# Kernel tuning notes

Measured on AMD Instinct MI355X. Metric: run time of the kernel, lower is better.

Reference implementation:

```python
import jax, jax.numpy as jnp
import numpy as np
from jax import lax

# PRPN (Parse-Read-Predict Network), eval mode (all dropout off, BatchNorm in eval
# with running stats mean=0/var=1, rmask=ones). Submodule math follows the upstream
# yikangshen/PRPN implementation vendored by jiant: ParsingNetwork (conv gate stack,
# hard hardtanh memory gates with cumprod over slots), ReadingNetwork (masked-softmax
# attention over nslots memory + LayerNorm LSTM cell, shift-append memory update),
# PredictNetwork (attention over prediction memory, res=0 -> Linear+BN+Tanh head).

T, B, V, D, H, S, L, NL = 192, 32, 50000, 384, 384, 15, 5, 2
RES = 0.1
G4 = 4 * H
BN_SC = np.float32(1.0 / np.sqrt(1.0 + 1e-5))   # eval BatchNorm with mean=0, var=1
INV_SQRT_H = np.float32(1.0 / np.sqrt(H))


def _layer_norm(x, g, b, eps=1e-6):
    # torch-style LayerNorm with unbiased std (x.std(-1))
    mu = jnp.mean(x, -1, keepdims=True)
    var = jnp.sum((x - mu) ** 2, -1, keepdims=True) / (x.shape[-1] - 1)
    return g * (x - mu) / (jnp.sqrt(var) + eps) + b


def _msoftmax(logits, gate, eps=1e-8):
    # blocks.softmax: exp-normalize then multiply by (soft) gate mask before sum
    e = jnp.exp(logits - jnp.max(logits, -1, keepdims=True)) * gate
    return e / (jnp.sum(e, -1, keepdims=True) + eps)


def _forward(input_ids, emb_w, pconv1_w, pconv1_b, pbn_g, pbn_b, pconv2_w, pconv2_b,
             r_wih, r_bih, r_whh, r_bhh, r_lnih_g, r_lnih_b, r_lnhh_g, r_lnhh_b,
             r_lnc_g, r_lnc_b, r_proj_w, r_proj_b,
             p_proj_w, p_proj_b, p_ffd_w, p_ffd_b, p_bn_g, p_bn_b):
    emb = emb_w[input_ids]                                        # (T,B,D)

    # ---- ParsingNetwork ----
    x = jnp.concatenate([jnp.zeros((L, B, D), emb.dtype), emb], 0)  # (T+L,B,D), zero history
    xc = jnp.transpose(x, (1, 2, 0))                              # (B,D,T+L)
    h1 = lax.conv_general_dilated(xc, pconv1_w, (1,), 'VALID',
                                  dimension_numbers=('NCH', 'OIH', 'NCH'))
    h1 = h1 + pconv1_b[None, :, None]
    h1 = jax.nn.relu(pbn_g[None, :, None] * h1 * BN_SC + pbn_b[None, :, None])  # (B,H,T)
    half = H // 2
    # Conv1d(nhid, 2, 1, groups=2): channel 0 from first half, channel 1 from second
    gate = jax.nn.sigmoid(jnp.einsum('bct,c->bt', h1[:, :half], pconv2_w[0]) + pconv2_b[0])
    gate_next = jax.nn.sigmoid(jnp.einsum('bct,c->bt', h1[:, half:], pconv2_w[1]) + pconv2_b[1])
    cum = jnp.concatenate([jnp.full((B, S), 1e9, gate.dtype), gate], 1)  # init cum_gate = +inf
    gate_hat = jnp.stack([cum[:, S - k:S - k + T] for k in range(S)], 2)  # (B,T,S)

    def mem_gate(g):  # hard gates: (hardtanh((g-ghat)/res*2+1)+1)/2, cumprod over slots
        u = (jnp.clip((g[:, :, None] - gate_hat) / RES * 2.0 + 1.0, -1.0, 1.0) + 1.0) * 0.5
        return jnp.cumprod(u, axis=2)

    mg = jnp.transpose(mem_gate(gate), (1, 0, 2))                 # (T,B,S)
    mgn = jnp.transpose(mem_gate(gate_next), (1, 0, 2))           # (T,B,S)

    # ---- per-timestep Read / Predict-attention loop ----
    def step(carry, xs):
        mem_h, mem_c, pmem = carry       # (NL,B,S,H),(NL,B,S,H),(B,S,H)
        e_t, mg_t, mgn_t = xs
        h = e_t
        nh, nc = [], []
        for j in range(NL):
            mh, mc = mem_h[j], mem_c[j]
            key_j = jnp.concatenate([h, mh[:, -1]], -1) @ r_proj_w[j].T + r_proj_b[j]
            att = _msoftmax(jnp.einsum('bsh,bh->bs', mh, key_j) * INV_SQRT_H, mg_t)
            sel_h = jnp.einsum('bs,bsh->bh', att, mh)
            sel_c = jnp.einsum('bs,bsh->bh', att, mc)
            gates = (_layer_norm(h @ r_wih[j].T + r_bih[j], r_lnih_g[j], r_lnih_b[j])
                     + _layer_norm(sel_h @ r_whh[j].T + r_bhh[j], r_lnhh_g[j], r_lnhh_b[j]))
            i_g, f_g, c_g, o_g = jnp.split(gates, 4, axis=-1)
            c_new = jax.nn.sigmoid(f_g) * sel_c + jax.nn.sigmoid(i_g) * jnp.tanh(c_g)
            h_new = jax.nn.sigmoid(o_g) * jnp.tanh(_layer_norm(c_new, r_lnc_g[j], r_lnc_b[j]))
            nh.append(jnp.concatenate([mh[:, 1:], h_new[:, None]], 1))
            nc.append(jnp.concatenate([mc[:, 1:], c_new[:, None]], 1))
            h = h_new
        pkey = jnp.concatenate([h, pmem[:, -1]], -1) @ p_proj_w.T + p_proj_b
        patt = _msoftmax(jnp.einsum('bsh,bh->bs', pmem, pkey) * INV_SQRT_H, mgn_t)
        sel = jnp.einsum('bs,bsh->bh', patt, pmem)
        pmem_new = jnp.concatenate([pmem[:, 1:], h[:, None]], 1)
        return (jnp.stack(nh), jnp.stack(nc), pmem_new), (h, sel)

    carry0 = (jnp.zeros((NL, B, S, H), emb.dtype),
              jnp.zeros((NL, B, S, H), emb.dtype),
              jnp.zeros((B, S, H), emb.dtype))
    _, (out_h, out_sel) = lax.scan(step, carry0, (emb, mg, mgn))

    # ---- PredictNetwork head (res=0): Linear(2H->D) + BN(eval) + Tanh ----
    flat = jnp.concatenate([out_h.reshape(T * B, H), out_sel.reshape(T * B, H)], -1)
    y = flat @ p_ffd_w.T + p_ffd_b
    y = jnp.tanh(p_bn_g * y * BN_SC + p_bn_b)
    return y.reshape(T, B, D)


def setup_inputs() -> dict:
    key = jax.random.key(0)
    ks = iter(jax.random.split(key, 16))

    def rn(shape, s=0.05):
        return jax.random.normal(next(ks), shape, dtype=jnp.float32) * s

    return {
        "input_ids": jax.random.randint(next(ks), (T, B), 0, V),
        "emb_w": rn((V, D), 0.01),
        "pconv1_w": rn((H, D, L + 1)),
        "pconv1_b": jnp.zeros((H,), jnp.float32),
        "pbn_g": jnp.ones((H,), jnp.float32),
        "pbn_b": jnp.zeros((H,), jnp.float32),
        "pconv2_w": rn((2, H // 2)),
        "pconv2_b": jnp.zeros((2,), jnp.float32),
        "r_wih": rn((NL, G4, D)),
        "r_bih": jnp.zeros((NL, G4), jnp.float32),
        "r_whh": rn((NL, G4, H)),
        "r_bhh": jnp.zeros((NL, G4), jnp.float32),
        "r_lnih_g": jnp.ones((NL, G4), jnp.float32),
        "r_lnih_b": jnp.zeros((NL, G4), jnp.float32),
        "r_lnhh_g": jnp.ones((NL, G4), jnp.float32),
        "r_lnhh_b": jnp.zeros((NL, G4), jnp.float32),
        "r_lnc_g": jnp.ones((NL, H), jnp.float32),
        "r_lnc_b": jnp.zeros((NL, H), jnp.float32),
        "r_proj_w": rn((NL, H, D + H)),
        "r_proj_b": jnp.zeros((NL, H), jnp.float32),
        "p_proj_w": rn((H, 2 * H)),
        "p_proj_b": jnp.zeros((H,), jnp.float32),
        "p_ffd_w": rn((D, 2 * H)),
        "p_ffd_b": jnp.zeros((D,), jnp.float32),
        "p_bn_g": jnp.ones((D,), jnp.float32),
        "p_bn_b": jnp.zeros((D,), jnp.float32),
    }


def reference(input_ids, emb_w, pconv1_w, pconv1_b, pbn_g, pbn_b, pconv2_w, pconv2_b,
              r_wih, r_bih, r_whh, r_bhh, r_lnih_g, r_lnih_b, r_lnhh_g, r_lnhh_b,
              r_lnc_g, r_lnc_b, r_proj_w, r_proj_b,
              p_proj_w, p_proj_b, p_ffd_w, p_ffd_b, p_bn_g, p_bn_b):
    out = _forward(input_ids, emb_w, pconv1_w, pconv1_b, pbn_g, pbn_b, pconv2_w, pconv2_b,
                   r_wih, r_bih, r_whh, r_bhh, r_lnih_g, r_lnih_b, r_lnhh_g, r_lnhh_b,
                   r_lnc_g, r_lnc_b, r_proj_w, r_proj_b,
                   p_proj_w, p_proj_b, p_ffd_w, p_ffd_b, p_bn_g, p_bn_b)
    mask = input_ids != 0
    return out, mask
```

## Files before the change

### kernel.cpp

```cpp
#include <hip/hip_runtime.h>


#define TT 192
#define TB 6144

constexpr size_t O_EMB    = 0;
constexpr size_t O_IH0LN  = 2359296;
constexpr size_t O_KEY0E  = 11796480;
constexpr size_t O_MG     = 14155776;
constexpr size_t O_MGN    = 14247936;
constexpr size_t O_H1     = 14340096;
constexpr size_t O_P0S    = 14340096;
constexpr size_t O_P1S    = 14389248;
constexpr size_t O_IH1RAW = 14438400;
constexpr size_t O_KEY1H  = 14536704;
constexpr size_t O_KEY0MH = 14561280;
constexpr size_t O_KEY1MH = 14573568;
constexpr size_t O_PKEYH  = 14585856;
constexpr size_t O_PKEYMH = 14610432;
constexpr size_t O_HNEW0  = 14635008;
constexpr size_t O_HNEW1  = 14647296;
constexpr size_t O_BAR    = 14671872;
constexpr size_t O_DEADEND= 14675968;
constexpr size_t O_GATEA  = 16699392;
constexpr size_t O_GATEB  = 16705536;
constexpr size_t O_OUTHS  = 16711680;
constexpr size_t O_MEMH0  = 21430272;
constexpr size_t O_MEMC0  = 21614592;
constexpr size_t O_MEMH1  = 21798912;
constexpr size_t O_MEMC1  = 21983232;
constexpr size_t O_PMEM   = 22167552;
constexpr size_t O_P0     = 22351872;
constexpr size_t O_P1     = 23089152;
constexpr size_t O_STATEEND = 23826432;

#define L0F 0
#define L1F 512
#define PRF 1024
#define G0F 1536
#define G1F 3072

__device__ __forceinline__ float sigmoidf(float x) { return 1.f / (1.f + expf(-x)); }

__device__ __forceinline__ float ldx(const float* p) {
  return __hip_atomic_load(p, __ATOMIC_RELAXED, __HIP_MEMORY_SCOPE_AGENT);
}
__device__ __forceinline__ void stx(float* p, float v) {
  __hip_atomic_store(p, v, __ATOMIC_RELAXED, __HIP_MEMORY_SCOPE_AGENT);
}
__device__ __forceinline__ float2 ldx2(const float* p) {
  unsigned long long v = __hip_atomic_load((const unsigned long long*)p,
                                           __ATOMIC_RELAXED, __HIP_MEMORY_SCOPE_AGENT);
  return __builtin_bit_cast(float2, v);
}
__device__ __forceinline__ void stx2(float* p, float2 v) {
  __hip_atomic_store((unsigned long long*)p, __builtin_bit_cast(unsigned long long, v),
                     __ATOMIC_RELAXED, __HIP_MEMORY_SCOPE_AGENT);
}
__device__ __forceinline__ int ldi(const int* p) {
  return __hip_atomic_load(p, __ATOMIC_RELAXED, __HIP_MEMORY_SCOPE_AGENT);
}
__device__ __forceinline__ void sti(int* p, int v) {
  __hip_atomic_store(p, v, __ATOMIC_RELAXED, __HIP_MEMORY_SCOPE_AGENT);
}

constexpr float BN_SC = 0.9999950000374997f;
constexpr float INV_SQRT_H = 0.05103103630798288f;

__device__ __forceinline__ float blockSum(float v, float* red) {
#pragma unroll
  for (int off = 32; off > 0; off >>= 1) v += __shfl_down(v, off, 64);
  __syncthreads();
  if ((threadIdx.x & 63) == 0) red[threadIdx.x >> 6] = v;
  __syncthreads();
  return red[0] + red[1] + red[2] + red[3];
}

__device__ __forceinline__ float2 wred2(float a, float b) {
#pragma unroll
  for (int off = 32; off > 0; off >>= 1) {
    a += __shfl_xor(a, off, 64);
    b += __shfl_xor(b, off, 64);
  }
  return make_float2(a, b);
}

__global__ __launch_bounds__(256) void k_zero(float* p, int n) {
  int i = blockIdx.x * 256 + threadIdx.x;
  int stride = gridDim.x * 256;
  for (; i < n; i += stride) p[i] = 0.f;
}

__global__ __launch_bounds__(256) void k_emb(const int* ids, const float* emb_w,
                                             float* emb, float* out) {
  size_t idx = (size_t)blockIdx.x * 256 + threadIdx.x;
  size_t stride = (size_t)gridDim.x * 256;
  for (size_t i = idx; i < (size_t)TB * 384; i += stride) {
    size_t tb = i / 384, d = i - tb * 384;
    int id = ids[tb];
    emb[i] = emb_w[(size_t)id * 384 + d];
    if (i < TB) out[(size_t)TB * 384 + i] = (ids[i] != 0) ? 1.f : 0.f;
  }
}

__global__ __launch_bounds__(256) void k_conv(const float* emb, const float* W1, const float* cbias,
                                              const float* bng, const float* bnb, float* h1) {
  __shared__ float As[32][68];
  __shared__ float Bs[32][68];
  int n0 = blockIdx.x * 64, m0 = blockIdx.y * 64;
  int tid = threadIdx.x;
  float acc[4][4] = {};
  int mi = tid >> 3, kq = tid & 7;
  int ni = tid >> 2, kb = tid & 3;
  for (int kk = 0; kk < 2304; kk += 32) {
    int kc = kk / 384, dbase = kk - kc * 384;
    __syncthreads();
#pragma unroll
    for (int p = 0; p < 2; ++p) {
      int m = m0 + mi + 32 * p;
      int b = m / 192, t = m - b * 192;
      int tt = t + kc - 5;
      float4 v = {0.f, 0.f, 0.f, 0.f};
      if (tt >= 0) v = *(const float4*)(emb + ((size_t)tt * 32 + b) * 384 + dbase + kq * 4);
      As[kq * 4 + 0][mi + 32 * p] = v.x; As[kq * 4 + 1][mi + 32 * p] = v.y;
      As[kq * 4 + 2][mi + 32 * p] = v.z; As[kq * 4 + 3][mi + 32 * p] = v.w;
    }
#pragma unroll
    for (int i = 0; i < 8; ++i) {
      int d = dbase + kb * 8 + i;
      Bs[kb * 8 + i][ni] = W1[(size_t)(n0 + ni) * 2304 + d * 6 + kc];
    }
    __syncthreads();
    int ty = tid >> 4, tx = tid & 15;
#pragma unroll
    for (int k = 0; k < 32; ++k) {
      float4 a = *(const float4*)(&As[k][ty * 4]);
      float4 bv = *(const float4*)(&Bs[k][tx * 4]);
      acc[0][0] += a.x * bv.x; acc[0][1] += a.x * bv.y; acc[0][2] += a.x * bv.z; acc[0][3] += a.x * bv.w;
      acc[1][0] += a.y * bv.x; acc[1][1] += a.y * bv.y; acc[1][2] += a.y * bv.z; acc[1][3] += a.y * bv.w;
      acc[2][0] += a.z * bv.x; acc[2][1] += a.z * bv.y; acc[2][2] += a.z * bv.z; acc[2][3] += a.z * bv.w;
      acc[3][0] += a.w * bv.x; acc[3][1] += a.w * bv.y; acc[3][2] += a.w * bv.z; acc[3][3] += a.w * bv.w;
    }
  }
  int ty = tid >> 4, tx = tid & 15;
#pragma unroll
  for (int i = 0; i < 4; ++i) {
    int m = m0 + ty * 4 + i;
#pragma unroll
    for (int j = 0; j < 4; ++j) {
      int n = n0 + tx * 4 + j;
      float v = acc[i][j] + cbias[n];
      v = bng[n] * v * BN_SC + bnb[n];
      h1[(size_t)m * 384 + n] = fmaxf(v, 0.f);
    }
  }
}

__global__ __launch_bounds__(256) void k_gate(const float* h1, const float* w2, const float* b2,
                                              float* gA, float* gB) {
  __shared__ float red[8];
  int bt = blockIdx.x, tid = threadIdx.x;
  float v0 = 0.f, v1 = 0.f;
  if (tid < 192) {
    v0 = h1[(size_t)bt * 384 + tid] * w2[tid];
    v1 = h1[(size_t)bt * 384 + 192 + tid] * w2[192 + tid];
  }
  float s0 = blockSum(v0, red);
  float s1 = blockSum(v1, red);
  if (tid == 0) {
    gA[bt] = 1.f / (1.f + expf(-(s0 + b2[0])));
    gB[bt] = 1.f / (1.f + expf(-(s1 + b2[1])));
  }
}

__global__ __launch_bounds__(256) void k_mg(const float* gA, const float* gB, float* mg, float* mgn) {
  int idx = blockIdx.x * 256 + threadIdx.x;
  if (idx >= TB) return;
  int t = idx >> 5, b = idx & 31;
  float g = gA[b * 192 + t], gn = gB[b * 192 + t];
  float p = 1.f, pn = 1.f;
  for (int k = 0; k < 15; ++k) {
    float ghat = (k <= t) ? gA[b * 192 + t - k] : 1e9f;
    float u = fminf(fmaxf((g - ghat) / 0.1f * 2.f + 1.f, -1.f), 1.f);
    float un = fminf(fmaxf((gn - ghat) / 0.1f * 2.f + 1.f, -1.f), 1.f);
    p *= (u + 1.f) * 0.5f;
    pn *= (un + 1.f) * 0.5f;
    mg[(size_t)idx * 15 + k] = p;
    mgn[(size_t)idx * 15 + k] = pn;
  }
}

__global__ __launch_bounds__(256) void k_gemm(const float* A, int lda, const float* W, int ldw,
                                              const float* bias, float* Cf, int ldc, int K, int mode,
                                              const float* bng, const float* bnb, float* Cb) {
  __shared__ float As[32][68];
  __shared__ float Bs[32][68];
  int n0 = blockIdx.x * 64, m0 = blockIdx.y * 64;
  int tid = threadIdx.x;
  float acc[4][4] = {};
  int mi = tid >> 3, kq = tid & 7;
  int ni = tid >> 2, kb = tid & 3;
  for (int kk = 0; kk < K; kk += 32) {
    __syncthreads();
#pragma unroll
    for (int p = 0; p < 2; ++p) {
      int m = m0 + mi + 32 * p;
      float4 v = *(const float4*)(A + (size_t)m * lda + kk + kq * 4);
      As[kq * 4 + 0][mi + 32 * p] = v.x; As[kq * 4 + 1][mi + 32 * p] = v.y;
      As[kq * 4 + 2][mi + 32 * p] = v.z; As[kq * 4 + 3][mi + 32 * p] = v.w;
    }
    {
      const float* wp = W + (size_t)(n0 + ni) * ldw + kk + kb * 8;
      float4 q0 = *(const float4*)(wp);
      float4 q1 = *(const float4*)(wp + 4);
      Bs[kb * 8 + 0][ni] = q0.x; Bs[kb * 8 + 1][ni] = q0.y;
      Bs[kb * 8 + 2][ni] = q0.z; Bs[kb * 8 + 3][ni] = q0.w;
      Bs[kb * 8 + 4][ni] = q1.x; Bs[kb * 8 + 5][ni] = q1.y;
      Bs[kb * 8 + 6][ni] = q1.z; Bs[kb * 8 + 7][ni] = q1.w;
    }
    __syncthreads();
    int ty = tid >> 4, tx = tid & 15;
#pragma unroll
    for (int k = 0; k < 32; ++k) {
      float4 a = *(const float4*)(&As[k][ty * 4]);
      float4 bv = *(const float4*)(&Bs[k][tx * 4]);
      acc[0][0] += a.x * bv.x; acc[0][1] += a.x * bv.y; acc[0][2] += a.x * bv.z; acc[0][3] += a.x * bv.w;
      acc[1][0] += a.y * bv.x; acc[1][1] += a.y * bv.y; acc[1][2] += a.y * bv.z; acc[1][3] += a.y * bv.w;
      acc[2][0] += a.z * bv.x; acc[2][1] += a.z * bv.y; acc[2][2] += a.z * bv.z; acc[2][3] += a.z * bv.w;
      acc[3][0] += a.w * bv.x; acc[3][1] += a.w * bv.y; acc[3][2] += a.w * bv.z; acc[3][3] += a.w * bv.w;
    }
  }
  int ty = tid >> 4, tx = tid & 15;
#pragma unroll
  for (int i = 0; i < 4; ++i) {
    int m = m0 + ty * 4 + i;
#pragma unroll
    for (int j = 0; j < 4; ++j) {
      int n = n0 + tx * 4 + j;
      float v = acc[i][j];
      if (bias) v += bias[n];
      if (mode == 0) Cf[(size_t)m * ldc + n] = v;
      else Cb[(size_t)m * ldc + n] = tanhf(bng[n] * v * BN_SC + bnb[n]);
    }
  }
}

__global__ __launch_bounds__(256) void k_ln_rows(float* X, const float* g, const float* bt) {
  __shared__ float red[8];
  float* x = X + (size_t)blockIdx.x * 1536;
  int tid = threadIdx.x;
  float ps = 0.f;
  for (int i = tid; i < 1536; i += 256) ps += x[i];
  float mu = blockSum(ps, red) * (1.f / 1536.f);
  ps = 0.f;
  for (int i = tid; i < 1536; i += 256) { float d = x[i] - mu; ps += d * d; }
  float inv = 1.f / (sqrtf(blockSum(ps, red) * (1.f / 1535.f)) + 1e-6f);
  for (int i = tid; i < 1536; i += 256) x[i] = g[i] * (x[i] - mu) * inv + bt[i];
}

struct ScanArgs {
  float* ws;
  const float *r_whh, *r_bhh, *r_lnhh_g, *r_lnhh_b, *r_lnih_g, *r_lnih_b;
  const float *r_lnc_g, *r_lnc_b, *r_wih, *r_bih, *r_proj_w, *r_proj_b;
  const float *p_proj_w, *p_proj_b;
};

struct GJob { const float* W; int ldw; int koff; const float* bias; float* dst; int rstride; int ncols; };

__device__ __forceinline__ void resolveJob(const GJob* J, int col, const float*& W, int& ldw, int& koff,
                                           const float*& bias, float*& dst, int& rstride, int& cc) {
  int c = col;
#pragma unroll
  for (int j = 0; j < 4; ++j) {
    if (c < J[j].ncols) {
      W = J[j].W; ldw = J[j].ldw; koff = J[j].koff; bias = J[j].bias;
      dst = J[j].dst; rstride = J[j].rstride; cc = c; return;
    }
    c -= J[j].ncols;
  }
  W = J[0].W; ldw = J[0].ldw; koff = J[0].koff; bias = J[0].bias;
  dst = J[0].dst; rstride = J[0].rstride; cc = 0;
}

__device__ __forceinline__ void stage_x(const float* src, float* xs) {
  const int tid = threadIdx.x;
  for (int j2 = tid; j2 < 6144; j2 += 256) {
    int j = j2 * 2;
    int bb = j / 384, kk = j - bb * 384;
    float2 v = ldx2(src + j);
    xs[bb * 385 + kk] = v.x; xs[bb * 385 + kk + 1] = v.y;
  }
}

__device__ void gemv_run(const GJob* J, int cbase, int ncols, const float* xs, float* red) {
  const int tid = threadIdx.x;
  const int b = tid & 31, cg = tid >> 5;
  float xr[48];
  const float* xp = xs + b * 385 + cg * 48;
#pragma unroll
  for (int q = 0; q < 48; ++q) xr[q] = xp[q];
  for (int ch = 0; ch < ncols; ch += 21) {
    const int nch = min(21, ncols - ch);
    for (int ci = 0; ci < nch; ++ci) {
      const float* W; int ldw, koff; const float* bias; float* dst; int rstride; int cc;
      resolveJob(J, cbase + ch + ci, W, ldw, koff, bias, dst, rstride, cc);
      const float* wr = W + (size_t)cc * ldw + koff + cg * 48;
      float a = 0.f;
#pragma unroll
      for (int q = 0; q < 12; ++q) {
        float4 w = *(const float4*)(wr + q * 4);
        a += w.x * xr[q * 4 + 0] + w.y * xr[q * 4 + 1]
           + w.z * xr[q * 4 + 2] + w.w * xr[q * 4 + 3];
      }
      a += __shfl_down(a, 32, 64);
      if ((cg & 1) == 0) red[((cg >> 1) * nch + ci) * 33 + b] = a;
    }
    __syncthreads();
    const int pairs = nch * 32;
    for (int pi = tid; pi < pairs; pi += 256) {
      int bb = pi / nch, ci = pi - bb * nch;
      float s = red[(0 * nch + ci) * 33 + bb] + red[(1 * nch + ci) * 33 + bb]
              + red[(2 * nch + ci) * 33 + bb] + red[(3 * nch + ci) * 33 + bb];
      const float* W; int ldw, koff; const float* bias; float* dst; int rstride; int cc;
      resolveJob(J, cbase + ch + ci, W, ldw, koff, bias, dst, rstride, cc);
      if (bias) s += bias[cc];
      stx(dst + (size_t)bb * rstride + cc, s);
    }
    __syncthreads();
  }
}

__device__ __forceinline__ void wave_attn(const float* memh, const float* klds, const float* mgp,
                                          int t, int lane, float (&att)[15]) {
  const int g = lane >> 2, l = lane & 3;
  float part = 0.f;
  if (g < 15) {
    const float* mh = memh + ((t + g) % 15) * 384 + l;
#pragma unroll 8
    for (int k = 0; k < 96; ++k) part += mh[4 * k] * klds[l + 4 * k];
  }
  part += __shfl_xor(part, 1, 64);
  part += __shfl_xor(part, 2, 64);
  float logit[15];
#pragma unroll
  for (int s = 0; s < 15; ++s) logit[s] = __shfl(part, 4 * s, 64) * INV_SQRT_H;
  float m = logit[0];
#pragma unroll
  for (int s = 1; s < 15; ++s) m = fmaxf(m, logit[s]);
  float sum = 0.f;
#pragma unroll
  for (int s = 0; s < 15; ++s) { att[s] = expf(logit[s] - m) * mgp[s]; sum += att[s]; }
  float inv = 1.f / (sum + 1e-8f);
#pragma unroll
  for (int s = 0; s < 15; ++s) att[s] *= inv;
}

__device__ void l0_loop(int b, int lane, float* klds, const ScanArgs& A, int* bar) {
  float* ws = A.ws;
  float* memh = ws + O_MEMH0 + (size_t)b * 5760;
  float* memc = ws + O_MEMC0 + (size_t)b * 5760;
  float* mir  = ws + O_P0 + (size_t)b * 23040;
  const float* stg = ws + O_P0S + (size_t)b * 1536;
  const int* p1 = bar + G0F + lane * 16;
  const int* p2 = bar + G0F + (64 + (lane & 31)) * 16;
  for (int t = 0; t < 192; ++t) {
    const size_t tb = (size_t)t * 32 + b;
    float2 ih[12];
#pragma unroll
    for (int j = 0; j < 12; ++j)
      ih[j] = *(const float2*)(ws + O_IH0LN + tb * 1536 + 2 * lane + 128 * j);
    float2 kE[3];
#pragma unroll
    for (int j = 0; j < 3; ++j)
      kE[j] = *(const float2*)(ws + O_KEY0E + tb * 384 + 2 * lane + 128 * j);
    while (true) {
      int a = ldi(p1);
      int c = (lane < 32) ? ldi(p2) : 0x7fffffff;
      if (__all(a >= t && c >= t)) break;
      __builtin_amdgcn_s_sleep(1);
    }
    float2 fresh[12];
#pragma unroll
    for (int j = 0; j < 12; ++j) fresh[j] = ldx2(stg + 2 * lane + 128 * j);
#pragma unroll
    for (int j = 0; j < 3; ++j) {
      float2 c2 = ldx2(ws + O_KEY0MH + (size_t)b * 384 + 2 * lane + 128 * j);
      *(float2*)(klds + 2 * lane + 128 * j) = make_float2(kE[j].x + c2.x, kE[j].y + c2.y);
    }
    float att[15];
    wave_attn(memh, klds, ws + O_MG + tb * 15, t, lane, att);
    float2 acc[12];
#pragma unroll
    for (int j = 0; j < 12; ++j) {
      float2 bb = *(const float2*)(A.r_bhh + 2 * lane + 128 * j);
      acc[j] = make_float2(bb.x + att[14] * fresh[j].x, bb.y + att[14] * fresh[j].y);
    }
#pragma unroll
    for (int s = 0; s < 14; ++s) {
      const float* P = mir + ((t + s) % 15) * 1536;
      float a = att[s];
#pragma unroll
      for (int j = 0; j < 12; ++j) {
        float2 p = *(const float2*)(P + 2 * lane + 128 * j);
        acc[j].x += a * p.x; acc[j].y += a * p.y;
      }
    }
    float2 selc[3];
#pragma unroll
    for (int j = 0; j < 3; ++j) selc[j] = make_float2(0.f, 0.f);
#pragma unroll
    for (int s = 0; s < 15; ++s) {
      const float* C = memc + ((t + s) % 15) * 384;
      float a = att[s];
#pragma unroll
      for (int j = 0; j < 3; ++j) {
        float2 p = *(const float2*)(C + 2 * lane + 128 * j);
        selc[j].x += a * p.x; selc[j].y += a * p.y;
      }
    }
    float s1 = 0.f, s2 = 0.f;
#pragma unroll
    for (int j = 0; j < 12; ++j) {
      s1 += acc[j].x + acc[j].y;
      s2 += acc[j].x * acc[j].x + acc[j].y * acc[j].y;
    }
    float2 r = wred2(s1, s2);
    float mu = r.x * (1.f / 1536.f);
    float inv = 1.f / (sqrtf(fmaxf(r.y - r.x * mu, 0.f) * (1.f / 1535.f)) + 1e-6f);
    const float* hg = A.r_lnhh_g;
    const float* hb = A.r_lnhh_b;
    float2 cn[3], og[3];
#pragma unroll
    for (int jj = 0; jj < 3; ++jj) {
      const int d = 2 * lane + 128 * jj;
      float2 gi, gf, gc, go;
      { float2 g2 = *(const float2*)(hg + d), b2 = *(const float2*)(hb + d);
        gi.x = ih[jj].x + g2.x * (acc[jj].x - mu) * inv + b2.x;
        gi.y = ih[jj].y + g2.y * (acc[jj].y - mu) * inv + b2.y; }
      { float2 g2 = *(const float2*)(hg + 384 + d), b2 = *(const float2*)(hb + 384 + d);
        gf.x = ih[3 + jj].x + g2.x * (acc[3 + jj].x - mu) * inv + b2.x;
        gf.y = ih[3 + jj].y + g2.y * (acc[3 + jj].y - mu) * inv + b2.y; }
      { float2 g2 = *(const float2*)(hg + 768 + d), b2 = *(const float2*)(hb + 768 + d);
        gc.x = ih[6 + jj].x + g2.x * (acc[6 + jj].x - mu) * inv + b2.x;
        gc.y = ih[6 + jj].y + g2.y * (acc[6 + jj].y - mu) * inv + b2.y; }
      { float2 g2 = *(const float2*)(hg + 1152 + d), b2 = *(const float2*)(hb + 1152 + d);
        go.x = ih[9 + jj].x + g2.x * (acc[9 + jj].x - mu) * inv + b2.x;
        go.y = ih[9 + jj].y + g2.y * (acc[9 + jj].y - mu) * inv + b2.y; }
      cn[jj].x = sigmoidf(gf.x) * selc[jj].x + sigmoidf(gi.x) * tanhf(gc.x);
      cn[jj].y = sigmoidf(gf.y) * selc[jj].y + sigmoidf(gi.y) * tanhf(gc.y);
      og[jj] = go;
    }
    s1 = 0.f; s2 = 0.f;
#pragma unroll
    for (int jj = 0; jj < 3; ++jj) {
      s1 += cn[jj].x + cn[jj].y;
      s2 += cn[jj].x * cn[jj].x + cn[jj].y * cn[jj].y;
    }
    r = wred2(s1, s2);
    float mu_c = r.x * (1.f / 384.f);
    float inv_c = 1.f / (sqrtf(fmaxf(r.y - r.x * mu_c, 0.f) * (1.f / 383.f)) + 1e-6f);
    const int slot = t % 15;
    const int pslot = (t + 14) % 15;
#pragma unroll
    for (int jj = 0; jj < 3; ++jj) {
      const int d = 2 * lane + 128 * jj;
      float2 lg2 = *(const float2*)(A.r_lnc_g + d), lb2 = *(const float2*)(A.r_lnc_b + d);
      float2 hn;
      hn.x = sigmoidf(og[jj].x) * tanhf(lg2.x * (cn[jj].x - mu_c) * inv_c + lb2.x);
      hn.y = sigmoidf(og[jj].y) * tanhf(lg2.y * (cn[jj].y - mu_c) * inv_c + lb2.y);
      *(float2*)(memh + slot * 384 + d) = hn;
      *(float2*)(memc + slot * 384 + d) = cn[jj];
      stx2(ws + O_HNEW0 + (size_t)b * 384 + d, hn);
    }
#pragma unroll
    for (int j = 0; j < 12; ++j)
      *(float2*)(mir + pslot * 1536 + 2 * lane + 128 * j) = fresh[j];
    asm volatile("s_waitcnt vmcnt(0)" ::: "memory");
    if (lane == 0) sti(bar + L0F + b * 16, t + 1);
  }
}

__device__ void l1_loop(int b, int lane, float* klds, const ScanArgs& A, int* bar) {
  float* ws = A.ws;
  float* memh = ws + O_MEMH1 + (size_t)b * 5760;
  float* memc = ws + O_MEMC1 + (size_t)b * 5760;
  float* mir  = ws + O_P1 + (size_t)b * 23040;
  const float* stg = ws + O_P1S + (size_t)b * 1536;
  const float* hg = A.r_lnhh_g + 1536;
  const float* hb = A.r_lnhh_b + 1536;
  const float* igp = A.r_lnih_g + 1536;
  const float* ibp = A.r_lnih_b + 1536;
  const float* bhh = A.r_bhh + 1536;
  const float* lcg = A.r_lnc_g + 384;
  const float* lcb = A.r_lnc_b + 384;
  const int* p1 = bar + G0F + lane * 16;
  const int* p2 = bar + G0F + (64 + (lane & 31)) * 16;
  const int* p3 = bar + G1F + lane * 16;
  for (int t = 0; t < 192; ++t) {
    while (true) {
      int a = ldi(p1);
      int c = (lane < 32) ? ldi(p2) : 0x7fffffff;
      int d2 = ldi(p3);
      if (__all(a >= t + 1 && c >= t + 1 && d2 >= t)) break;
      __builtin_amdgcn_s_sleep(1);
    }
    const size_t tb = (size_t)t * 32 + b;
    const size_t par = (size_t)(t & 1);
    float2 gx[12], fresh[12];
#pragma unroll
    for (int j = 0; j < 12; ++j) {
      gx[j] = ldx2(ws + O_IH1RAW + par * 49152 + (size_t)b * 1536 + 2 * lane + 128 * j);
      fresh[j] = ldx2(stg + 2 * lane + 128 * j);
    }
#pragma unroll
    for (int j = 0; j < 3; ++j) {
      float2 a2 = ldx2(ws + O_KEY1H + par * 12288 + (size_t)b * 384 + 2 * lane + 128 * j);
      float2 c2 = ldx2(ws + O_KEY1MH + (size_t)b * 384 + 2 * lane + 128 * j);
      *(float2*)(klds + 2 * lane + 128 * j) = make_float2(a2.x + c2.x, a2.y + c2.y);
    }
    float att[15];
    wave_attn(memh, klds, ws + O_MG + tb * 15, t, lane, att);
    float2 acc[12];
#pragma unroll
    for (int j = 0; j < 12; ++j) {
      float2 bb = *(const float2*)(bhh + 2 * lane + 128 * j);
      acc[j] = make_float2(bb.x + att[14] * fresh[j].x, bb.y + att[14] * fresh[j].y);
    }
#pragma unroll
    for (int s = 0; s < 14; ++s) {
      const float* P = mir + ((t + s) % 15) * 1536;
      float a = att[s];
#pragma unroll
      for (int j = 0; j < 12; ++j) {
        float2 p = *(const float2*)(P + 2 * lane + 128 * j);
        acc[j].x += a * p.x; acc[j].y += a * p.y;
      }
    }
    float2 selc[3];
#pragma unroll
    for (int j = 0; j < 3; ++j) selc[j] = make_float2(0.f, 0.f);
#pragma unroll
    for (int s = 0; s < 15; ++s) {
      const float* C = memc + ((t + s) % 15) * 384;
      float a = att[s];
#pragma unroll
      for (int j = 0; j < 3; ++j) {
        float2 p = *(const float2*)(C + 2 * lane + 128 * j);
        selc[j].x += a * p.x; selc[j].y += a * p.y;
      }
    }
    float s1 = 0.f, s2 = 0.f;
#pragma unroll
    for (int j = 0; j < 12; ++j) {
      s1 += gx[j].x + gx[j].y;
      s2 += gx[j].x * gx[j].x + gx[j].y * gx[j].y;
    }
    float2 r = wred2(s1, s2);
    float mu_i = r.x * (1.f / 1536.f);
    float inv_i = 1.f / (sqrtf(fmaxf(r.y - r.x * mu_i, 0.f) * (1.f / 1535.f)) + 1e-6f);
    s1 = 0.f; s2 = 0.f;
#pragma unroll
    for (int j = 0; j < 12; ++j) {
      s1 += acc[j].x + acc[j].y;
      s2 += acc[j].x * acc[j].x + acc[j].y * acc[j].y;
    }
    r = wred2(s1, s2);
    float mu = r.x * (1.f / 1536.f);
    float inv = 1.f / (sqrtf(fmaxf(r.y - r.x * mu, 0.f) * (1.f / 1535.f)) + 1e-6f);
    float2 cn[3], og[3];
#pragma unroll
    for (int jj = 0; jj < 3; ++jj) {
      const int d = 2 * lane + 128 * jj;
      float2 gi, gf, gc, go;
      { float2 i2 = *(const float2*)(igp + d), ib2 = *(const float2*)(ibp + d);
        float2 g2 = *(const float2*)(hg + d), b2 = *(const float2*)(hb + d);
        gi.x = i2.x * (gx[jj].x - mu_i) * inv_i + ib2.x + g2.x * (acc[jj].x - mu) * inv + b2.x;
        gi.y = i2.y * (gx[jj].y - mu_i) * inv_i + ib2.y + g2.y * (acc[jj].y - mu) * inv + b2.y; }
      { float2 i2 = *(const float2*)(igp + 384 + d), ib2 = *(const float2*)(ibp + 384 + d);
        float2 g2 = *(const float2*)(hg + 384 + d), b2 = *(const float2*)(hb + 384 + d);
        gf.x = i2.x * (gx[3 + jj].x - mu_i) * inv_i + ib2.x + g2.x * (acc[3 + jj].x - mu) * inv + b2.x;
        gf.y = i2.y * (gx[3 + jj].y - mu_i) * inv_i + ib2.y + g2.y * (acc[3 + jj].y - mu) * inv + b2.y; }
      { float2 i2 = *(const float2*)(igp + 768 + d), ib2 = *(const float2*)(ibp + 768 + d);
        float2 g2 = *(const float2*)(hg + 768 + d), b2 = *(const float2*)(hb + 768 + d);
        gc.x = i2.x * (gx[6 + jj].x - mu_i) * inv_i + ib2.x + g2.x * (acc[6 + jj].x - mu) * inv + b2.x;
        gc.y = i2.y * (gx[6 + jj].y - mu_i) * inv_i + ib2.y + g2.y * (acc[6 + jj].y - mu) * inv + b2.y; }
      { float2 i2 = *(const float2*)(igp + 1152 + d), ib2 = *(const float2*)(ibp + 1152 + d);
        float2 g2 = *(const float2*)(hg + 1152 + d), b2 = *(const float2*)(hb + 1152 + d);
        go.x = i2.x * (gx[9 + jj].x - mu_i) * inv_i + ib2.x + g2.x * (acc[9 + jj].x - mu) * inv + b2.x;
        go.y = i2.y * (gx[9 + jj].y - mu_i) * inv_i + ib2.y + g2.y * (acc[9 + jj].y - mu) * inv + b2.y; }
      cn[jj].x = sigmoidf(gf.x) * selc[jj].x + sigmoidf(gi.x) * tanhf(gc.x);
      cn[jj].y = sigmoidf(gf.y) * selc[jj].y + sigmoidf(gi.y) * tanhf(gc.y);
      og[jj] = go;
    }
    s1 = 0.f; s2 = 0.f;
#pragma unroll
    for (int jj = 0; jj < 3; ++jj) {
      s1 += cn[jj].x + cn[jj].y;
      s2 += cn[jj].x * cn[jj].x + cn[jj].y * cn[jj].y;
    }
    r = wred2(s1, s2);
    float mu_c = r.x * (1.f / 384.f);
    float inv_c = 1.f / (sqrtf(fmaxf(r.y - r.x * mu_c, 0.f) * (1.f / 383.f)) + 1e-6f);
    const int slot = t % 15;
    const int pslot = (t + 14) % 15;
#pragma unroll
    for (int jj = 0; jj < 3; ++jj) {
      const int d = 2 * lane + 128 * jj;
      float2 lg2 = *(const float2*)(lcg + d), lb2 = *(const float2*)(lcb + d);
      float2 hn;
      hn.x = sigmoidf(og[jj].x) * tanhf(lg2.x * (cn[jj].x - mu_c) * inv_c + lb2.x);
      hn.y = sigmoidf(og[jj].y) * tanhf(lg2.y * (cn[jj].y - mu_c) * inv_c + lb2.y);
      *(float2*)(memh + slot * 384 + d) = hn;
      *(float2*)(memc + slot * 384 + d) = cn[jj];
      stx2(ws + O_HNEW1 + par * 12288 + (size_t)b * 384 + d, hn);
      *(float2*)(ws + O_OUTHS + tb * 768 + d) = hn;
    }
#pragma unroll
    for (int j = 0; j < 12; ++j)
      *(float2*)(mir + pslot * 1536 + 2 * lane + 128 * j) = fresh[j];
    asm volatile("s_waitcnt vmcnt(0)" ::: "memory");
    if (lane == 0) sti(bar + L1F + b * 16, t + 1);
  }
}

__device__ void pr_loop(int b, int lane, float* klds, const ScanArgs& A, int* bar) {
  float* ws = A.ws;
  float* pmem = ws + O_PMEM + (size_t)b * 5760;
  const int* p1 = bar + G1F + lane * 16;
  for (int t = 0; t < 192; ++t) {
    while (true) {
      int a = ldi(p1);
      if (__all(a >= t + 1)) break;
      __builtin_amdgcn_s_sleep(1);
    }
    const size_t tb = (size_t)t * 32 + b;
#pragma unroll
    for (int j = 0; j < 3; ++j) {
      float2 a2 = ldx2(ws + O_PKEYH + (size_t)(t & 1) * 12288 + (size_t)b * 384 + 2 * lane + 128 * j);
      float2 c2 = ldx2(ws + O_PKEYMH + (size_t)((t + 1) & 1) * 12288 + (size_t)b * 384 + 2 * lane + 128 * j);
      *(float2*)(klds + 2 * lane + 128 * j) = make_float2(a2.x + c2.x, a2.y + c2.y);
    }
    float att[15];
    wave_attn(pmem, klds, ws + O_MGN + tb * 15, t, lane, att);
    float2 sel[3];
#pragma unroll
    for (int j = 0; j < 3; ++j) sel[j] = make_float2(0.f, 0.f);
#pragma unroll
    for (int s = 0; s < 15; ++s) {
      const float* P = pmem + ((t + s) % 15) * 384;
      float a = att[s];
#pragma unroll
      for (int j = 0; j < 3; ++j) {
        float2 p = *(const float2*)(P + 2 * lane + 128 * j);
        sel[j].x += a * p.x; sel[j].y += a * p.y;
      }
    }
#pragma unroll
    for (int j = 0; j < 3; ++j)
      *(float2*)(ws + O_OUTHS + tb * 768 + 384 + 2 * lane + 128 * j) = sel[j];
#pragma unroll
    for (int j = 0; j < 3; ++j) {
      float2 v = ldx2(ws + O_HNEW1 + (size_t)(t & 1) * 12288 + (size_t)b * 384 + 2 * lane + 128 * j);
      *(float2*)(pmem + (t % 15) * 384 + 2 * lane + 128 * j) = v;
    }
    asm volatile("s_waitcnt vmcnt(0)" ::: "memory");
    if (lane == 0) sti(bar + PRF + b * 16, t + 1);
  }
}

__device__ void g0_loop(int gwg, const ScanArgs& A, int* bar, float* sm) {
  float* ws = A.ws;
  const int tid = threadIdx.x;
  float* xs = sm;
  float* red = sm + 12320;
  const int cbase = gwg * 40;
  for (int t = 0; t < 192; ++t) {
    if (tid < 64) {
      const int* p = (tid < 32) ? (bar + L0F + tid * 16) : (bar + L1F + (tid - 32) * 16);
      const int tgt = (tid < 32) ? (t + 1) : (t - 1);
      while (true) {
        int v = ldi(p);
        if (__all(v >= tgt)) break;
        __builtin_amdgcn_s_sleep(1);
      }
    }
    __syncthreads();
    stage_x(ws + O_HNEW0, xs);
    __syncthreads();
    const size_t par = (size_t)(t & 1);
    GJob J[4] = {
      { A.r_wih + 589824, 384, 0, A.r_bih + 1536, ws + O_IH1RAW + par * 49152, 1536, 1536 },
      { A.r_proj_w + 294912, 768, 0, A.r_proj_b + 384, ws + O_KEY1H + par * 12288, 384, 384 },
      { A.r_whh, 384, 0, nullptr, ws + O_P0S, 1536, 1536 },
      { A.r_proj_w, 768, 384, nullptr, ws + O_KEY0MH, 384, 384 },
    };
    gemv_run(J, cbase, 40, xs, red);
    if (tid == 0) sti(bar + G0F + gwg * 16, t + 1);
  }
}

__device__ void g1_loop(int gwg, const ScanArgs& A, int* bar, float* sm) {
  float* ws = A.ws;
  const int tid = threadIdx.x;
  float* xs = sm;
  float* red = sm + 12320;
  const int cbase = gwg * 42;
  for (int t = 0; t < 192; ++t) {
    if (tid < 64) {
      const int* p = (tid < 32) ? (bar + L1F + tid * 16) : (bar + PRF + (tid - 32) * 16);
      const int tgt = (tid < 32) ? (t + 1) : t;
      while (true) {
        int v = ldi(p);
        if (__all(v >= tgt)) break;
        __builtin_amdgcn_s_sleep(1);
      }
    }
    __syncthreads();
    const size_t par = (size_t)(t & 1);
    stage_x(ws + O_HNEW1 + par * 12288, xs);
    __syncthreads();
    GJob J[4] = {
      { A.r_whh + 589824, 384, 0, nullptr, ws + O_P1S, 1536, 1536 },
      { A.r_proj_w + 294912, 768, 384, nullptr, ws + O_KEY1MH, 384, 384 },
      { A.p_proj_w, 768, 0, A.p_proj_b, ws + O_PKEYH + par * 12288, 384, 384 },
      { A.p_proj_w, 768, 384, nullptr, ws + O_PKEYMH + par * 12288, 384, 384 },
    };
    gemv_run(J, cbase, 42, xs, red);
    if (tid == 0) sti(bar + G1F + gwg * 16, t + 1);
  }
}

__global__ __launch_bounds__(256) void k_scan(ScanArgs A) {
  __shared__ float sm[15104];
  int* bar = (int*)(A.ws + O_BAR);
  const int wg = blockIdx.x;
  const int tid = threadIdx.x;
  const int lane = tid & 63;
  const int wv = tid >> 6;
  if (wg < 8)        l0_loop(wg * 4 + wv, lane, sm + wv * 384, A, bar);
  else if (wg < 16)  l1_loop((wg - 8) * 4 + wv, lane, sm + wv * 384, A, bar);
  else if (wg < 24)  pr_loop((wg - 16) * 4 + wv, lane, sm + wv * 384, A, bar);
  else if (wg < 120) g0_loop(wg - 24, A, bar, sm);
  else               g1_loop(wg - 120, A, bar, sm);
}

extern "C" void kernel_launch(void* const* d_in, const int* in_sizes, int n_in,
                              void* d_out, int out_size, void* d_ws, size_t ws_size,
                              hipStream_t stream) {
  const int* ids = (const int*)d_in[0];
  const float* emb_w = (const float*)d_in[1];
  const float* pconv1_w = (const float*)d_in[2];
  const float* pconv1_b = (const float*)d_in[3];
  const float* pbn_g = (const float*)d_in[4];
  const float* pbn_b = (const float*)d_in[5];
  const float* pconv2_w = (const float*)d_in[6];
  const float* pconv2_b = (const float*)d_in[7];
  const float* r_wih = (const float*)d_in[8];
  const float* r_bih = (const float*)d_in[9];
  const float* r_whh = (const float*)d_in[10];
  const float* r_bhh = (const float*)d_in[11];
  const float* r_lnih_g = (const float*)d_in[12];
  const float* r_lnih_b = (const float*)d_in[13];
  const float* r_lnhh_g = (const float*)d_in[14];
  const float* r_lnhh_b = (const float*)d_in[15];
  const float* r_lnc_g = (const float*)d_in[16];
  const float* r_lnc_b = (const float*)d_in[17];
  const float* r_proj_w = (const float*)d_in[18];
  const float* r_proj_b = (const float*)d_in[19];
  const float* p_proj_w = (const float*)d_in[20];
  const float* p_proj_b = (const float*)d_in[21];
  const float* p_ffd_w = (const float*)d_in[22];
  const float* p_ffd_b = (const float*)d_in[23];
  const float* p_bn_g = (const float*)d_in[24];
  const float* p_bn_b = (const float*)d_in[25];
  float* ws = (float*)d_ws;
  float* out = (float*)d_out;

  k_zero<<<1024, 256, 0, stream>>>(ws + O_MEMH0, (int)(O_STATEEND - O_MEMH0));
  k_emb<<<4096, 256, 0, stream>>>(ids, emb_w, ws + O_EMB, out);
  k_conv<<<dim3(6, 96), 256, 0, stream>>>(ws + O_EMB, pconv1_w, pconv1_b, pbn_g, pbn_b, ws + O_H1);
  k_gate<<<6144, 256, 0, stream>>>(ws + O_H1, pconv2_w, pconv2_b, ws + O_GATEA, ws + O_GATEB);
  k_mg<<<24, 256, 0, stream>>>(ws + O_GATEA, ws + O_GATEB, ws + O_MG, ws + O_MGN);
  k_zero<<<328, 256, 0, stream>>>(ws + O_P0S, (int)(O_DEADEND - O_P0S));
  k_gemm<<<dim3(24, 96), 256, 0, stream>>>(ws + O_EMB, 384, r_wih, 384, r_bih,
                                           ws + O_IH0LN, 1536, 384, 0, nullptr, nullptr, nullptr);
  k_gemm<<<dim3(6, 96), 256, 0, stream>>>(ws + O_EMB, 384, r_proj_w, 768, r_proj_b,
                                          ws + O_KEY0E, 384, 384, 0, nullptr, nullptr, nullptr);
  k_ln_rows<<<6144, 256, 0, stream>>>(ws + O_IH0LN, r_lnih_g, r_lnih_b);
  ScanArgs SA{ws, r_whh, r_bhh, r_lnhh_g, r_lnhh_b, r_lnih_g, r_lnih_b,
              r_lnc_g, r_lnc_b, r_wih, r_bih, r_proj_w, r_proj_b, p_proj_w, p_proj_b};
  k_scan<<<184, 256, 0, stream>>>(SA);
  k_gemm<<<dim3(6, 96), 256, 0, stream>>>(ws + O_OUTHS, 768, p_ffd_w, 768, p_ffd_b,
                                          nullptr, 384, 768, 1, p_bn_g, p_bn_b, out);
}
```

Before: 13.02 ms.

## Split recurrent GEMV workgroups by batch group with finer-grained dependency flags

```diff
diff --git a/kernel.cpp b/kernel.cpp
--- a/kernel.cpp
+++ b/kernel.cpp
@@ -34,11 +34,11 @@
 constexpr size_t O_P1     = 23089152;
 constexpr size_t O_STATEEND = 23826432;
 
-#define L0F 0
-#define L1F 512
-#define PRF 1024
-#define G0F 1536
-#define G1F 3072
+#define F_L0  0
+#define F_L1  32
+#define F_PR  64
+#define F_G0  96
+#define F_G1  192
 
 __device__ __forceinline__ float sigmoidf(float x) { return 1.f / (1.f + expf(-x)); }
 
@@ -282,51 +282,51 @@
   dst = J[0].dst; rstride = J[0].rstride; cc = 0;
 }
 
-__device__ __forceinline__ void stage_x(const float* src, float* xs) {
+__device__ __forceinline__ void stage_x8(const float* src, float* xs) {
   const int tid = threadIdx.x;
-  for (int j2 = tid; j2 < 6144; j2 += 256) {
-    int j = j2 * 2;
-    int bb = j / 384, kk = j - bb * 384;
-    float2 v = ldx2(src + j);
-    xs[bb * 385 + kk] = v.x; xs[bb * 385 + kk + 1] = v.y;
-  }
-}
-
-__device__ void gemv_run(const GJob* J, int cbase, int ncols, const float* xs, float* red) {
-  const int tid = threadIdx.x;
-  const int b = tid & 31, cg = tid >> 5;
-  float xr[48];
-  const float* xp = xs + b * 385 + cg * 48;
-#pragma unroll
-  for (int q = 0; q < 48; ++q) xr[q] = xp[q];
-  for (int ch = 0; ch < ncols; ch += 21) {
-    const int nch = min(21, ncols - ch);
-    for (int ci = 0; ci < nch; ++ci) {
-      const float* W; int ldw, koff; const float* bias; float* dst; int rstride; int cc;
-      resolveJob(J, cbase + ch + ci, W, ldw, koff, bias, dst, rstride, cc);
-      const float* wr = W + (size_t)cc * ldw + koff + cg * 48;
-      float a = 0.f;
-#pragma unroll
-      for (int q = 0; q < 12; ++q) {
-        float4 w = *(const float4*)(wr + q * 4);
-        a += w.x * xr[q * 4 + 0] + w.y * xr[q * 4 + 1]
-           + w.z * xr[q * 4 + 2] + w.w * xr[q * 4 + 3];
+  for (int jj = tid; jj < 1536; jj += 256) {
+    int j = jj * 2;
+    int bl = j / 384, k = j - bl * 384;
+    float2 v = ldx2(src + bl * 384 + k);
+    xs[bl * 388 + k] = v.x; xs[bl * 388 + k + 1] = v.y;
+  }
+}
+
+__device__ void gemv2(const GJob* J, int c0, int ncols, int gbb ,
+                      int kg, const float* xr) {
+  for (int ci = 0; ci < ncols; ci += 2) {
+    const float *W0, *W1; int ldw0, ldw1, ko0, ko1; const float *bs0, *bs1;
+    float *d0, *d1; int rs0, rs1, cc0, cc1;
+    resolveJob(J, c0 + ci, W0, ldw0, ko0, bs0, d0, rs0, cc0);
+    resolveJob(J, c0 + ci + 1, W1, ldw1, ko1, bs1, d1, rs1, cc1);
+    const float* wr0 = W0 + (size_t)cc0 * ldw0 + ko0 + kg * 48;
+    const float* wr1 = W1 + (size_t)cc1 * ldw1 + ko1 + kg * 48;
+    float a0 = 0.f, a1 = 0.f, b0 = 0.f, b1 = 0.f;
+#pragma unroll
+    for (int q = 0; q < 6; ++q) {
+      float4 wA = *(const float4*)(wr0 + q * 8);
+      float4 wB = *(const float4*)(wr0 + q * 8 + 4);
+      a0 += wA.x * xr[q * 8 + 0] + wA.y * xr[q * 8 + 1] + wA.z * xr[q * 8 + 2] + wA.w * xr[q * 8 + 3];
+      b0 += wB.x * xr[q * 8 + 4] + wB.y * xr[q * 8 + 5] + wB.z * xr[q * 8 + 6] + wB.w * xr[q * 8 + 7];
+      float4 wC = *(const float4*)(wr1 + q * 8);
+      float4 wD = *(const float4*)(wr1 + q * 8 + 4);
+      a1 += wC.x * xr[q * 8 + 0] + wC.y * xr[q * 8 + 1] + wC.z * xr[q * 8 + 2] + wC.w * xr[q * 8 + 3];
+      b1 += wD.x * xr[q * 8 + 4] + wD.y * xr[q * 8 + 5] + wD.z * xr[q * 8 + 6] + wD.w * xr[q * 8 + 7];
+    }
+    a0 += b0; a1 += b1;
+    a0 += __shfl_xor(a0, 1, 64); a1 += __shfl_xor(a1, 1, 64);
+    a0 += __shfl_xor(a0, 2, 64); a1 += __shfl_xor(a1, 2, 64);
+    a0 += __shfl_xor(a0, 4, 64); a1 += __shfl_xor(a1, 4, 64);
+    if (kg == 0) {
+      if (bs0) a0 += bs0[cc0];
+      if (bs1) a1 += bs1[cc1];
+      if (d0 == d1 && rs0 == rs1 && cc1 == cc0 + 1) {
+        stx2(d0 + (size_t)gbb * rs0 + cc0, make_float2(a0, a1));
+      } else {
+        stx(d0 + (size_t)gbb * rs0 + cc0, a0);
+        stx(d1 + (size_t)gbb * rs1 + cc1, a1);
       }
-      a += __shfl_down(a, 32, 64);
-      if ((cg & 1) == 0) red[((cg >> 1) * nch + ci) * 33 + b] = a;
-    }
-    __syncthreads();
-    const int pairs = nch * 32;
-    for (int pi = tid; pi < pairs; pi += 256) {
-      int bb = pi / nch, ci = pi - bb * nch;
-      float s = red[(0 * nch + ci) * 33 + bb] + red[(1 * nch + ci) * 33 + bb]
-              + red[(2 * nch + ci) * 33 + bb] + red[(3 * nch + ci) * 33 + bb];
-      const float* W; int ldw, koff; const float* bias; float* dst; int rstride; int cc;
-      resolveJob(J, cbase + ch + ci, W, ldw, koff, bias, dst, rstride, cc);
-      if (bias) s += bias[cc];
-      stx(dst + (size_t)bb * rstride + cc, s);
-    }
-    __syncthreads();
+    }
   }
 }
 
@@ -361,8 +361,7 @@
   float* memc = ws + O_MEMC0 + (size_t)b * 5760;
   float* mir  = ws + O_P0 + (size_t)b * 23040;
   const float* stg = ws + O_P0S + (size_t)b * 1536;
-  const int* p1 = bar + G0F + lane * 16;
-  const int* p2 = bar + G0F + (64 + (lane & 31)) * 16;
+  const int bg = b >> 3;
   for (int t = 0; t < 192; ++t) {
     const size_t tb = (size_t)t * 32 + b;
     float2 ih[12];
@@ -373,11 +372,9 @@
 #pragma unroll
     for (int j = 0; j < 3; ++j)
       kE[j] = *(const float2*)(ws + O_KEY0E + tb * 384 + 2 * lane + 128 * j);
-    while (true) {
-      int a = ldi(p1);
-      int c = (lane < 32) ? ldi(p2) : 0x7fffffff;
-      if (__all(a >= t && c >= t)) break;
-      __builtin_amdgcn_s_sleep(1);
+    if (lane < 24) {
+      const int* fp = bar + F_G0 + lane * 4 + bg;
+      while (ldi(fp) < t) __builtin_amdgcn_s_sleep(1);
     }
     float2 fresh[12];
 #pragma unroll
@@ -476,7 +473,7 @@
     for (int j = 0; j < 12; ++j)
       *(float2*)(mir + pslot * 1536 + 2 * lane + 128 * j) = fresh[j];
     asm volatile("s_waitcnt vmcnt(0)" ::: "memory");
-    if (lane == 0) sti(bar + L0F + b * 16, t + 1);
+    if (lane == 0) sti(bar + F_L0 + b, t + 1);
   }
 }
 
@@ -493,16 +490,14 @@
   const float* bhh = A.r_bhh + 1536;
   const float* lcg = A.r_lnc_g + 384;
   const float* lcb = A.r_lnc_b + 384;
-  const int* p1 = bar + G0F + lane * 16;
-  const int* p2 = bar + G0F + (64 + (lane & 31)) * 16;
-  const int* p3 = bar + G1F + lane * 16;
+  const int bg = b >> 3;
   for (int t = 0; t < 192; ++t) {
-    while (true) {
-      int a = ldi(p1);
-      int c = (lane < 32) ? ldi(p2) : 0x7fffffff;
-      int d2 = ldi(p3);
-      if (__all(a >= t + 1 && c >= t + 1 && d2 >= t)) break;
-      __builtin_amdgcn_s_sleep(1);
+    if (lane < 37) {
+      const int* fp; int tgt;
+      if (lane < 24)      { fp = bar + F_G0 + lane * 4 + bg;        tgt = t + 1; }
+      else if (lane < 36) { fp = bar + F_G1 + (lane - 24) * 4 + bg; tgt = t; }
+      else                { fp = bar + F_PR + b;                    tgt = t - 1; }
+      while (ldi(fp) < tgt) __builtin_amdgcn_s_sleep(1);
     }
     const size_t tb = (size_t)t * 32 + b;
     const size_t par = (size_t)(t & 1);
@@ -619,19 +614,18 @@
     for (int j = 0; j < 12; ++j)
       *(float2*)(mir + pslot * 1536 + 2 * lane + 128 * j) = fresh[j];
     asm volatile("s_waitcnt vmcnt(0)" ::: "memory");
-    if (lane == 0) sti(bar + L1F + b * 16, t + 1);
+    if (lane == 0) sti(bar + F_L1 + b, t + 1);
   }
 }
 
 __device__ void pr_loop(int b, int lane, float* klds, const ScanArgs& A, int* bar) {
   float* ws = A.ws;
   float* pmem = ws + O_PMEM + (size_t)b * 5760;
-  const int* p1 = bar + G1F + lane * 16;
+  const int bg = b >> 3;
   for (int t = 0; t < 192; ++t) {
-    while (true) {
-      int a = ldi(p1);
-      if (__all(a >= t + 1)) break;
-      __builtin_amdgcn_s_sleep(1);
+    if (lane < 12) {
+      const int* fp = bar + F_G1 + lane * 4 + bg;
+      while (ldi(fp) < t + 1) __builtin_amdgcn_s_sleep(1);
     }
     const size_t tb = (size_t)t * 32 + b;
 #pragma unroll
@@ -664,29 +658,34 @@
       *(float2*)(pmem + (t % 15) * 384 + 2 * lane + 128 * j) = v;
     }
     asm volatile("s_waitcnt vmcnt(0)" ::: "memory");
-    if (lane == 0) sti(bar + PRF + b * 16, t + 1);
-  }
-}
-
-__device__ void g0_loop(int gwg, const ScanArgs& A, int* bar, float* sm) {
+    if (lane == 0) sti(bar + F_PR + b, t + 1);
+  }
+}
+
+__device__ void g0_loop(int cg, int bg, const ScanArgs& A, int* bar, float* sm) {
   float* ws = A.ws;
   const int tid = threadIdx.x;
+  const int lane = tid & 63, wv = tid >> 6;
+  const int bl = lane >> 3, kg = lane & 7;
+  const int gb = bg * 8;
   float* xs = sm;
-  float* red = sm + 12320;
-  const int cbase = gwg * 40;
+  const int c0 = cg * 160 + wv * 40;
   for (int t = 0; t < 192; ++t) {
-    if (tid < 64) {
-      const int* p = (tid < 32) ? (bar + L0F + tid * 16) : (bar + L1F + (tid - 32) * 16);
-      const int tgt = (tid < 32) ? (t + 1) : (t - 1);
-      while (true) {
-        int v = ldi(p);
-        if (__all(v >= tgt)) break;
-        __builtin_amdgcn_s_sleep(1);
-      }
-    }
-    __syncthreads();
-    stage_x(ws + O_HNEW0, xs);
-    __syncthreads();
+    if (tid < 16) {
+      const int* fp; int tgt;
+      if (tid < 8) { fp = bar + F_L0 + gb + tid;     tgt = t + 1; }
+      else         { fp = bar + F_L1 + gb + tid - 8; tgt = t - 1; }
+      while (ldi(fp) < tgt) __builtin_amdgcn_s_sleep(1);
+    }
+    __syncthreads();
+    stage_x8(ws + O_HNEW0 + (size_t)gb * 384, xs);
+    __syncthreads();
+    float xr[48];
+    {
+      const float* xp = xs + bl * 388 + kg * 48;
+#pragma unroll
+      for (int q = 0; q < 48; ++q) xr[q] = xp[q];
+    }
     const size_t par = (size_t)(t & 1);
     GJob J[4] = {
       { A.r_wih + 589824, 384, 0, A.r_bih + 1536, ws + O_IH1RAW + par * 49152, 1536, 1536 },
@@ -694,44 +693,51 @@
       { A.r_whh, 384, 0, nullptr, ws + O_P0S, 1536, 1536 },
       { A.r_proj_w, 768, 384, nullptr, ws + O_KEY0MH, 384, 384 },
     };
-    gemv_run(J, cbase, 40, xs, red);
-    if (tid == 0) sti(bar + G0F + gwg * 16, t + 1);
-  }
-}
-
-__device__ void g1_loop(int gwg, const ScanArgs& A, int* bar, float* sm) {
+    gemv2(J, c0, 40, gb + bl, kg, xr);
+    __syncthreads();
+    if (tid == 0) sti(bar + F_G0 + cg * 4 + bg, t + 1);
+  }
+}
+
+__device__ void g1_loop(int cg, int bg, const ScanArgs& A, int* bar, float* sm) {
   float* ws = A.ws;
   const int tid = threadIdx.x;
+  const int lane = tid & 63, wv = tid >> 6;
+  const int bl = lane >> 3, kg = lane & 7;
+  const int gb = bg * 8;
   float* xs = sm;
-  float* red = sm + 12320;
-  const int cbase = gwg * 42;
+  const int c0 = cg * 224 + wv * 56;
   for (int t = 0; t < 192; ++t) {
-    if (tid < 64) {
-      const int* p = (tid < 32) ? (bar + L1F + tid * 16) : (bar + PRF + (tid - 32) * 16);
-      const int tgt = (tid < 32) ? (t + 1) : t;
-      while (true) {
-        int v = ldi(p);
-        if (__all(v >= tgt)) break;
-        __builtin_amdgcn_s_sleep(1);
-      }
+    if (tid < 16) {
+      const int* fp; int tgt;
+      if (tid < 8) { fp = bar + F_L1 + gb + tid;     tgt = t + 1; }
+      else         { fp = bar + F_PR + gb + tid - 8; tgt = t; }
+      while (ldi(fp) < tgt) __builtin_amdgcn_s_sleep(1);
     }
     __syncthreads();
     const size_t par = (size_t)(t & 1);
-    stage_x(ws + O_HNEW1 + par * 12288, xs);
-    __syncthreads();
+    stage_x8(ws + O_HNEW1 + par * 12288 + (size_t)gb * 384, xs);
+    __syncthreads();
+    float xr[48];
+    {
+      const float* xp = xs + bl * 388 + kg * 48;
+#pragma unroll
+      for (int q = 0; q < 48; ++q) xr[q] = xp[q];
+    }
     GJob J[4] = {
       { A.r_whh + 589824, 384, 0, nullptr, ws + O_P1S, 1536, 1536 },
       { A.r_proj_w + 294912, 768, 384, nullptr, ws + O_KEY1MH, 384, 384 },
       { A.p_proj_w, 768, 0, A.p_proj_b, ws + O_PKEYH + par * 12288, 384, 384 },
       { A.p_proj_w, 768, 384, nullptr, ws + O_PKEYMH + par * 12288, 384, 384 },
     };
-    gemv_run(J, cbase, 42, xs, red);
-    if (tid == 0) sti(bar + G1F + gwg * 16, t + 1);
+    gemv2(J, c0, 56, gb + bl, kg, xr);
+    __syncthreads();
+    if (tid == 0) sti(bar + F_G1 + cg * 4 + bg, t + 1);
   }
 }
 
 __global__ __launch_bounds__(256) void k_scan(ScanArgs A) {
-  __shared__ float sm[15104];
+  __shared__ float sm[3104];
   int* bar = (int*)(A.ws + O_BAR);
   const int wg = blockIdx.x;
   const int tid = threadIdx.x;
@@ -740,8 +746,8 @@
   if (wg < 8)        l0_loop(wg * 4 + wv, lane, sm + wv * 384, A, bar);
   else if (wg < 16)  l1_loop((wg - 8) * 4 + wv, lane, sm + wv * 384, A, bar);
   else if (wg < 24)  pr_loop((wg - 16) * 4 + wv, lane, sm + wv * 384, A, bar);
-  else if (wg < 120) g0_loop(wg - 24, A, bar, sm);
-  else               g1_loop(wg - 120, A, bar, sm);
+  else if (wg < 120) g0_loop((wg - 24) >> 2, (wg - 24) & 3, A, bar, sm);
+  else               g1_loop((wg - 120) >> 2, (wg - 120) & 3, A, bar, sm);
 }
 
 extern "C" void kernel_launch(void* const* d_in, const int* in_sizes, int n_in,
@@ -789,7 +795,7 @@
   k_ln_rows<<<6144, 256, 0, stream>>>(ws + O_IH0LN, r_lnih_g, r_lnih_b);
   ScanArgs SA{ws, r_whh, r_bhh, r_lnhh_g, r_lnhh_b, r_lnih_g, r_lnih_b,
               r_lnc_g, r_lnc_b, r_wih, r_bih, r_proj_w, r_proj_b, p_proj_w, p_proj_b};
-  k_scan<<<184, 256, 0, stream>>>(SA);
+  k_scan<<<168, 256, 0, stream>>>(SA);
   k_gemm<<<dim3(6, 96), 256, 0, stream>>>(ws + O_OUTHS, 768, p_ffd_w, 768, p_ffd_b,
                                           nullptr, 384, 768, 1, p_bn_g, p_bn_b, out);
 }
```

Measured after the change: 24.86 ms. +91.0%, slower.
